# Kernel optimization log

Hardware: AMD Instinct MI355X
Metric: run time of the kernel (lower is better)

The kernel has to match this reference:

```python
import jax, jax.numpy as jnp
import numpy as np

D_SCALE = 1000.0  # quantization scale for the int32 motion-magnitude depth key


def _forward_warp_max_motion(im0, flow, eps):
    """Depth-tested forward splatting (Sanchez et al. 2013, Alg. 3, max-motion variant).

    Each source pixel is bilinearly splatted to the 4 integer neighbors of its
    flow-displaced target. A scatter-max on quantized motion magnitude acts as the
    depth test; only contributions whose motion equals the per-pixel max are
    accumulated (deterministic two-pass version of the atomic CUDA kernel).
    """
    B, C, H, W = im0.shape
    fx, fy = flow[..., 0], flow[..., 1]
    x = jnp.arange(W, dtype=flow.dtype)[None, None, :] + fx  # [B,H,W] target x
    y = jnp.arange(H, dtype=flow.dtype)[None, :, None] + fy  # [B,H,W] target y
    x0 = jnp.floor(x)
    y0 = jnp.floor(y)
    ax = x - x0  # fractional parts -> bilinear weights
    ay = y - y0
    x0i = x0.astype(jnp.int32)
    y0i = y0.astype(jnp.int32)
    corners = [
        (x0i,     y0i,     (1.0 - ax) * (1.0 - ay)),
        (x0i + 1, y0i,     ax * (1.0 - ay)),
        (x0i,     y0i + 1, (1.0 - ax) * ay),
        (x0i + 1, y0i + 1, ax * ay),
    ]
    d = jnp.round(jnp.sqrt(fx * fx + fy * fy) * D_SCALE).astype(jnp.int32)  # [B,H,W]
    boff = (jnp.arange(B, dtype=jnp.int32) * (H * W))[:, None, None]
    idxs, ws, ds = [], [], []
    for tx, ty, w in corners:
        valid = (tx >= 0) & (tx < W) & (ty >= 0) & (ty < H)
        idx = jnp.where(valid, boff + ty * W + tx, 0)
        idxs.append(idx.reshape(-1))
        ws.append(jnp.where(valid, w, 0.0).reshape(-1))
        ds.append(jnp.where(valid, d, -1).reshape(-1))
    idx = jnp.concatenate(idxs)        # [4*B*H*W]
    wv = jnp.concatenate(ws)
    dv = jnp.concatenate(ds)
    N = B * H * W
    # pass 1: scatter-max depth buffer (init 0, as in the torch code)
    dbuf = jnp.zeros(N, jnp.int32).at[idx].max(dv)
    # pass 2: accumulate only depth-test winners
    win = (dv >= 0) & (dv == dbuf[idx])
    w_eff = jnp.where(win, wv, 0.0)
    wght = jnp.zeros(N, im0.dtype).at[idx].add(w_eff)  # kernel adds w per channel then /C == w once
    src = im0.transpose(1, 0, 2, 3).reshape(C, N)      # [C, N]
    vals = jnp.tile(src, (1, 4)) * w_eff[None, :]      # [C, 4N], corner-major matches idx
    im1buf = jnp.zeros((C, N), im0.dtype).at[:, idx].add(vals)
    wght_b = wght.reshape(B, 1, H, W)
    im1buf_b = im1buf.reshape(C, B, H, W).transpose(1, 0, 2, 3)
    im1 = im1buf_b / jnp.clip(wght_b, eps, None)
    disocclusions = (wght_b == 0).astype(im0.dtype)
    return im1, disocclusions, dbuf.reshape(B, 1, H, W)


def setup_inputs() -> dict:
    key = jax.random.key(0)
    k1, k2 = jax.random.split(key)
    B, C, H, W = 4, 3, 1080, 1920
    im0 = jax.random.uniform(k1, (B, C, H, W), dtype=jnp.float32)
    flow = jax.random.normal(k2, (B, H, W, 2), dtype=jnp.float32) * 20.0  # ~20 px motions
    return {"im0": im0, "flow": flow}


def reference(im0, flow):
    eps = 1e-05
    im1, _, _ = _forward_warp_max_motion(im0, flow, eps)
    return im1
```

## Files before the change

kernel.cpp:

```cpp
#include <hip/hip_runtime.h>

static constexpr int B = 4, C = 3, H = 1080, W = 1920;
static constexpr int HW = H * W;
static constexpr int NPIX = B * HW;
static constexpr int BLOCK = 256;

static constexpr int TW = 32, TH = 32;
static constexpr int TPX = TW * TH;
static constexpr int TXN = W / TW;
static constexpr int TYN = (H + TH - 1) / TH;
static constexpr int NT = TXN * TYN;
static constexpr int CAP = 1536;
static constexpr int OFL_CAP = 65536;
static constexpr int BPB = HW / BLOCK;

__device__ __forceinline__ int depth_key(float fx, float fy) {
    float m2 = __fadd_rn(__fmul_rn(fx, fx), __fmul_rn(fy, fy));
    return (int)rintf(__fmul_rn(sqrtf(m2), 1000.0f));
}

__global__ __launch_bounds__(BLOCK) void k_bin(const float2* __restrict__ flow,
                                               int* __restrict__ cnt,
                                               float4* __restrict__ bin,
                                               int* __restrict__ ofl_cnt,
                                               int* __restrict__ ofl_i,
                                               int* __restrict__ ofl_t,
                                               int* __restrict__ dbuf) {
    __shared__ int hcnt[NT];
    __shared__ int hbase[NT];
    const int tid = threadIdx.x;

    const int b = blockIdx.x / BPB;
    const int i = blockIdx.x * BLOCK + tid;
    const float2 f = flow[i];

    for (int j = tid; j < NT; j += BLOCK) hcnt[j] = 0;
    __syncthreads();

    const int pix = i - b * HW;
    const int h = pix / W;
    const int w = pix - h * W;
    const float x = (float)w + f.x;
    const float y = (float)h + f.y;
    const int x0 = (int)floorf(x);
    const int y0 = (int)floorf(y);
    const int d = depth_key(f.x, f.y);

    int tl[4], rk[4]; int ntl = 0;
    #pragma unroll
    for (int dy = 0; dy < 2; ++dy) {
        int cy = y0 + dy;
        if ((unsigned)cy >= (unsigned)H) continue;
        #pragma unroll
        for (int dx = 0; dx < 2; ++dx) {
            int cx = x0 + dx;
            if ((unsigned)cx >= (unsigned)W) continue;
            int t = (cy >> 5) * TXN + (cx >> 5);
            bool dup = false;
            for (int k = 0; k < ntl; ++k) dup |= (tl[k] == t);
            if (dup) continue;
            tl[ntl] = t;
            rk[ntl] = atomicAdd(&hcnt[t], 1);
            ++ntl;
        }
    }
    __syncthreads();

    for (int j = tid; j < NT; j += BLOCK) {
        int c = hcnt[j];
        if (c > 0) hbase[j] = atomicAdd(&cnt[b * NT + j], c);
    }
    __syncthreads();

    const float4 entry = make_float4(x, y, __int_as_float(pix), __int_as_float(d));
    bool did_depth_fb = false;
    for (int k = 0; k < ntl; ++k) {
        int t = tl[k];
        int slot = hbase[t] + rk[k];
        if (slot < CAP) {
            bin[(size_t)(b * NT + t) * CAP + slot] = entry;
        } else {
            int pos = atomicAdd(ofl_cnt, 1);
            if (pos < OFL_CAP) { ofl_i[pos] = i; ofl_t[pos] = t; }
            if (!did_depth_fb) {
                did_depth_fb = true;
                #pragma unroll
                for (int yy = 0; yy < 2; ++yy) {
                    int cy2 = y0 + yy;
                    if ((unsigned)cy2 >= (unsigned)H) continue;
                    #pragma unroll
                    for (int xx = 0; xx < 2; ++xx) {
                        int cx2 = x0 + xx;
                        if ((unsigned)cx2 >= (unsigned)W) continue;
                        atomicMax(&dbuf[b * HW + cy2 * W + cx2], d);
                    }
                }
            }
        }
    }
}

__global__ __launch_bounds__(BLOCK, 8) void k_tile(const float* __restrict__ im0,
                                                   const int* __restrict__ cnt,
                                                   const float4* __restrict__ bin,
                                                   const int* __restrict__ ofl_cnt,
                                                   int* __restrict__ dbuf,
                                                   float* __restrict__ wght,
                                                   float* __restrict__ out) {
    __shared__ int    dmax[TPX];
    __shared__ float4 accv[TPX];
    float* accf = (float*)accv;
    const int tid = threadIdx.x;
    const int bx = blockIdx.x, by = blockIdx.y, b = blockIdx.z;
    const int tx0 = bx * TW, ty0 = by * TH;
    const int t = by * TXN + bx;
    const bool have_ofl = (*ofl_cnt) > 0;
    int* db = dbuf + (size_t)b * HW;

    for (int i = tid; i < TPX; i += BLOCK) {
        int gy = ty0 + (i >> 5), gx = tx0 + (i & 31);
        dmax[i] = (have_ofl && gy < H) ? db[gy * W + gx] : 0;
        accv[i] = make_float4(0.0f, 0.0f, 0.0f, 0.0f);
    }
    __syncthreads();

    const int n = min(cnt[b * NT + t], CAP);
    const float4* mybin = bin + (size_t)(b * NT + t) * CAP;

    for (int e = tid; e < n; e += BLOCK) {
        float4 en = mybin[e];
        int x0 = (int)floorf(en.x);
        int y0 = (int)floorf(en.y);
        int d = __float_as_int(en.w);
        #pragma unroll
        for (int dy = 0; dy < 2; ++dy) {
            int cy = y0 + dy;
            if ((cy >> 5) != by || cy >= H) continue;
            #pragma unroll
            for (int dx = 0; dx < 2; ++dx) {
                int cx = x0 + dx;
                if ((cx >> 5) != bx) continue;
                atomicMax(&dmax[((cy - ty0) << 5) + (cx - tx0)], d);
            }
        }
    }
    __syncthreads();

    if (have_ofl) {
        for (int i = tid; i < TPX; i += BLOCK) {
            int gy = ty0 + (i >> 5), gx = tx0 + (i & 31);
            if (gy < H) db[gy * W + gx] = dmax[i];
        }
    }

    const float* ib = im0 + (size_t)b * C * HW;
    for (int e = tid; e < n; e += BLOCK) {
        float4 en = mybin[e];
        float x0f = floorf(en.x), y0f = floorf(en.y);
        int x0 = (int)x0f, y0 = (int)y0f;
        float ax = __fsub_rn(en.x, x0f);
        float ay = __fsub_rn(en.y, y0f);
        int pix = __float_as_int(en.z);
        int d   = __float_as_int(en.w);
        float wxv[2] = { __fsub_rn(1.0f, ax), ax };
        float wyv[2] = { __fsub_rn(1.0f, ay), ay };
        int   locs[4]; float lw[4]; int nw = 0;
        #pragma unroll
        for (int dy = 0; dy < 2; ++dy) {
            int cy = y0 + dy;
            if ((cy >> 5) != by || cy >= H) continue;
            #pragma unroll
            for (int dx = 0; dx < 2; ++dx) {
                int cx = x0 + dx;
                if ((cx >> 5) != bx) continue;
                int loc = ((cy - ty0) << 5) + (cx - tx0);
                if (dmax[loc] != d) continue;
                locs[nw] = loc;
                lw[nw] = __fmul_rn(wxv[dx], wyv[dy]);
                ++nw;
            }
        }
        if (nw) {
            float c0 = ib[pix];
            float c1 = ib[pix + HW];
            float c2 = ib[pix + 2 * HW];
            for (int k = 0; k < nw; ++k) {
                int p = locs[k]; float wg = lw[k];
                atomicAdd(&accf[4 * p + 0], wg);
                atomicAdd(&accf[4 * p + 1], __fmul_rn(c0, wg));
                atomicAdd(&accf[4 * p + 2], __fmul_rn(c1, wg));
                atomicAdd(&accf[4 * p + 3], __fmul_rn(c2, wg));
            }
        }
    }
    __syncthreads();

    float* ob = out + (size_t)b * C * HW;
    float* wb = wght + (size_t)b * HW;
    for (int i = tid; i < TPX; i += BLOCK) {
        int gy = ty0 + (i >> 5), gx = tx0 + (i & 31);
        if (gy >= H) continue;
        int g = gy * W + gx;
        float4 a = accv[i];
        if (have_ofl) {
            wb[g] = a.x;
            ob[g] = a.y; ob[g + HW] = a.z; ob[g + 2 * HW] = a.w;
        } else {
            float wv = fmaxf(a.x, 1e-5f);
            ob[g]          = __fdiv_rn(a.y, wv);
            ob[g + HW]     = __fdiv_rn(a.z, wv);
            ob[g + 2 * HW] = __fdiv_rn(a.w, wv);
        }
    }
}

__global__ __launch_bounds__(BLOCK) void k_accum_ofl(const float* __restrict__ im0,
                                                     const float2* __restrict__ flow,
                                                     const int* __restrict__ ofl_cnt,
                                                     const int* __restrict__ ofl_i,
                                                     const int* __restrict__ ofl_t,
                                                     const int* __restrict__ dbuf,
                                                     float* __restrict__ wght,
                                                     float* __restrict__ out) {
    int k = blockIdx.x * BLOCK + threadIdx.x;
    int n = min(*ofl_cnt, OFL_CAP);
    if (k >= n) return;
    int i = ofl_i[k], t = ofl_t[k];
    int b = i / HW;
    int pix = i - b * HW;
    int h = pix / W, w = pix - h * W;
    int bx = t % TXN, by = t / TXN;
    float2 f = flow[i];
    float x = (float)w + f.x;
    float y = (float)h + f.y;
    float x0f = floorf(x), y0f = floorf(y);
    int x0 = (int)x0f, y0 = (int)y0f;
    float ax = __fsub_rn(x, x0f);
    float ay = __fsub_rn(y, y0f);
    int d = depth_key(f.x, f.y);
    const float* src = im0 + (size_t)b * C * HW + pix;
    float c0 = src[0], c1 = src[HW], c2 = src[2 * HW];
    float wxv[2] = { __fsub_rn(1.0f, ax), ax };
    float wyv[2] = { __fsub_rn(1.0f, ay), ay };
    #pragma unroll
    for (int dy = 0; dy < 2; ++dy) {
        int cy = y0 + dy;
        if ((cy >> 5) != by || cy >= H) continue;
        #pragma unroll
        for (int dx = 0; dx < 2; ++dx) {
            int cx = x0 + dx;
            if ((cx >> 5) != bx) continue;
            int idx = b * HW + cy * W + cx;
            if (dbuf[idx] != d) continue;
            float wg = __fmul_rn(wxv[dx], wyv[dy]);
            atomicAdd(&wght[idx], wg);
            float* o = out + (size_t)b * C * HW + cy * W + cx;
            atomicAdd(&o[0],      __fmul_rn(c0, wg));
            atomicAdd(&o[HW],     __fmul_rn(c1, wg));
            atomicAdd(&o[2 * HW], __fmul_rn(c2, wg));
        }
    }
}

__global__ __launch_bounds__(BLOCK) void k_norm(float* __restrict__ out,
                                                const float* __restrict__ wght,
                                                const int* __restrict__ ofl_cnt) {
    if (*ofl_cnt == 0) return;
    for (int i = blockIdx.x * BLOCK + threadIdx.x; i < NPIX;
         i += gridDim.x * BLOCK) {
        int b = i / HW;
        int pix = i - b * HW;
        float wv = fmaxf(wght[i], 1e-5f);
        float* o = out + (size_t)b * C * HW + pix;
        o[0]      = __fdiv_rn(o[0], wv);
        o[HW]     = __fdiv_rn(o[HW], wv);
        o[2 * HW] = __fdiv_rn(o[2 * HW], wv);
    }
}

extern "C" void kernel_launch(void* const* d_in, const int* in_sizes, int n_in,
                              void* d_out, int out_size, void* d_ws, size_t ws_size,
                              hipStream_t stream) {
    const float*  im0  = (const float*)d_in[0];
    const float2* flow = (const float2*)d_in[1];
    float* out = (float*)d_out;

    char* ws = (char*)d_ws;
    float4* bin = (float4*)ws;
    const size_t bin_bytes = (size_t)B * NT * CAP * sizeof(float4);
    int*   dbuf    = (int*)(ws + bin_bytes);
    float* wght    = (float*)(ws + bin_bytes + (size_t)NPIX * 4);
    int*   cnt     = (int*)(ws + bin_bytes + (size_t)NPIX * 8);
    int*   ofl_cnt = cnt + B * NT;
    int*   ofl_i   = ofl_cnt + 1;
    int*   ofl_t   = ofl_i + OFL_CAP;

    hipMemsetAsync(dbuf, 0, (size_t)NPIX * 4, stream);
    hipMemsetAsync(cnt, 0, (size_t)(B * NT + 1) * 4, stream);

    int lgrid = NPIX / BLOCK;
    dim3 tgrid(TXN, TYN, B);

    k_bin      <<<lgrid, BLOCK, 0, stream>>>(flow, cnt, bin, ofl_cnt, ofl_i, ofl_t, dbuf);
    k_tile     <<<tgrid, BLOCK, 0, stream>>>(im0, cnt, bin, ofl_cnt, dbuf, wght, out);
    k_accum_ofl<<<OFL_CAP / BLOCK, BLOCK, 0, stream>>>(im0, flow, ofl_cnt, ofl_i, ofl_t, dbuf, wght, out);
    k_norm     <<<2048, BLOCK, 0, stream>>>(out, wght, ofl_cnt);
}
```

Measured before the change: 453.0 us.

## Process multiple pixels per thread in binning and register-cache tile entries

New measurement: 428.4 us. 1.06x faster.

```diff
diff --git a/kernel.cpp b/kernel.cpp
--- a/kernel.cpp
+++ b/kernel.cpp
@@ -11,12 +11,32 @@
 static constexpr int TYN = (H + TH - 1) / TH;
 static constexpr int NT = TXN * TYN;
 static constexpr int CAP = 1536;
+static constexpr int EPT = CAP / BLOCK;
 static constexpr int OFL_CAP = 65536;
-static constexpr int BPB = HW / BLOCK;
+
+static constexpr int PPT = 4;
+static constexpr int BPIX = BLOCK * PPT;
+static constexpr int BPB = HW / BPIX;
 
 __device__ __forceinline__ int depth_key(float fx, float fy) {
     float m2 = __fadd_rn(__fmul_rn(fx, fx), __fmul_rn(fy, fy));
     return (int)rintf(__fmul_rn(sqrtf(m2), 1000.0f));
+}
+
+__device__ __forceinline__ void merge_depth(int* __restrict__ dbuf, int bHW,
+                                            float x, float y, int d) {
+    int x0 = (int)floorf(x), y0 = (int)floorf(y);
+    #pragma unroll
+    for (int yy = 0; yy < 2; ++yy) {
+        int cy = y0 + yy;
+        if ((unsigned)cy >= (unsigned)H) continue;
+        #pragma unroll
+        for (int xx = 0; xx < 2; ++xx) {
+            int cx = x0 + xx;
+            if ((unsigned)cx >= (unsigned)W) continue;
+            atomicMax(&dbuf[bHW + cy * W + cx], d);
+        }
+    }
 }
 
 __global__ __launch_bounds__(BLOCK) void k_bin(const float2* __restrict__ flow,
@@ -29,40 +49,45 @@
     __shared__ int hcnt[NT];
     __shared__ int hbase[NT];
     const int tid = threadIdx.x;
-
     const int b = blockIdx.x / BPB;
-    const int i = blockIdx.x * BLOCK + tid;
-    const float2 f = flow[i];
+    const int gbase = blockIdx.x * BPIX + tid;
+
+    float2 f[PPT];
+    #pragma unroll
+    for (int k = 0; k < PPT; ++k) f[k] = flow[gbase + k * BLOCK];
 
     for (int j = tid; j < NT; j += BLOCK) hcnt[j] = 0;
     __syncthreads();
 
-    const int pix = i - b * HW;
-    const int h = pix / W;
-    const int w = pix - h * W;
-    const float x = (float)w + f.x;
-    const float y = (float)h + f.y;
-    const int x0 = (int)floorf(x);
-    const int y0 = (int)floorf(y);
-    const int d = depth_key(f.x, f.y);
-
-    int tl[4], rk[4]; int ntl = 0;
-    #pragma unroll
-    for (int dy = 0; dy < 2; ++dy) {
-        int cy = y0 + dy;
-        if ((unsigned)cy >= (unsigned)H) continue;
-        #pragma unroll
-        for (int dx = 0; dx < 2; ++dx) {
-            int cx = x0 + dx;
-            if ((unsigned)cx >= (unsigned)W) continue;
-            int t = (cy >> 5) * TXN + (cx >> 5);
-            bool dup = false;
-            for (int k = 0; k < ntl; ++k) dup |= (tl[k] == t);
-            if (dup) continue;
-            tl[ntl] = t;
-            rk[ntl] = atomicAdd(&hcnt[t], 1);
-            ++ntl;
-        }
+    float xs[PPT], ys[PPT];
+    int dd[PPT];
+    int ta[PPT], tb[PPT], tc[PPT], td[PPT];
+    int ra[PPT], rb[PPT], rc[PPT], rd[PPT];
+    #pragma unroll
+    for (int k = 0; k < PPT; ++k) {
+        const int i = gbase + k * BLOCK;
+        const int pix = i - b * HW;
+        const int h = pix / W;
+        const int w = pix - h * W;
+        const float x = (float)w + f[k].x;
+        const float y = (float)h + f[k].y;
+        xs[k] = x; ys[k] = y;
+        dd[k] = depth_key(f[k].x, f[k].y);
+        const int x0 = (int)floorf(x), y0 = (int)floorf(y);
+        const int x1 = x0 + 1, y1 = y0 + 1;
+        const bool vx0 = (unsigned)x0 < (unsigned)W, vx1 = (unsigned)x1 < (unsigned)W;
+        const bool vy0 = (unsigned)y0 < (unsigned)H, vy1 = (unsigned)y1 < (unsigned)H;
+        const int cx0 = x0 >> 5, cx1 = x1 >> 5;
+        const int cy0 = y0 >> 5, cy1 = y1 >> 5;
+        const bool dupx = (cx1 == cx0), dupy = (cy1 == cy0);
+        ta[k] = (vy0 && vx0)                   ? cy0 * TXN + cx0 : -1;
+        tb[k] = (vy0 && vx1 && !dupx)          ? cy0 * TXN + cx1 : -1;
+        tc[k] = (vy1 && vx0 && !dupy)          ? cy1 * TXN + cx0 : -1;
+        td[k] = (vy1 && vx1 && !dupx && !dupy) ? cy1 * TXN + cx1 : -1;
+        ra[k] = (ta[k] >= 0) ? atomicAdd(&hcnt[ta[k]], 1) : 0;
+        rb[k] = (tb[k] >= 0) ? atomicAdd(&hcnt[tb[k]], 1) : 0;
+        rc[k] = (tc[k] >= 0) ? atomicAdd(&hcnt[tc[k]], 1) : 0;
+        rd[k] = (td[k] >= 0) ? atomicAdd(&hcnt[td[k]], 1) : 0;
     }
     __syncthreads();
 
@@ -72,41 +97,42 @@
     }
     __syncthreads();
 
-    const float4 entry = make_float4(x, y, __int_as_float(pix), __int_as_float(d));
-    bool did_depth_fb = false;
-    for (int k = 0; k < ntl; ++k) {
-        int t = tl[k];
-        int slot = hbase[t] + rk[k];
-        if (slot < CAP) {
-            bin[(size_t)(b * NT + t) * CAP + slot] = entry;
-        } else {
-            int pos = atomicAdd(ofl_cnt, 1);
-            if (pos < OFL_CAP) { ofl_i[pos] = i; ofl_t[pos] = t; }
-            if (!did_depth_fb) {
-                did_depth_fb = true;
-                #pragma unroll
-                for (int yy = 0; yy < 2; ++yy) {
-                    int cy2 = y0 + yy;
-                    if ((unsigned)cy2 >= (unsigned)H) continue;
-                    #pragma unroll
-                    for (int xx = 0; xx < 2; ++xx) {
-                        int cx2 = x0 + xx;
-                        if ((unsigned)cx2 >= (unsigned)W) continue;
-                        atomicMax(&dbuf[b * HW + cy2 * W + cx2], d);
-                    }
-                }
-            }
-        }
-    }
-}
-
-__global__ __launch_bounds__(BLOCK, 8) void k_tile(const float* __restrict__ im0,
-                                                   const int* __restrict__ cnt,
-                                                   const float4* __restrict__ bin,
-                                                   const int* __restrict__ ofl_cnt,
-                                                   int* __restrict__ dbuf,
-                                                   float* __restrict__ wght,
-                                                   float* __restrict__ out) {
+    #pragma unroll
+    for (int k = 0; k < PPT; ++k) {
+        const int i = gbase + k * BLOCK;
+        const int pix = i - b * HW;
+        const float4 entry = make_float4(xs[k], ys[k],
+                                         __int_as_float(pix), __int_as_float(dd[k]));
+        bool fb = false;
+        #define EMIT(T, R)                                                     \
+            if ((T) >= 0) {                                                    \
+                int slot = hbase[T] + (R);                                     \
+                if (slot < CAP) {                                              \
+                    bin[(size_t)(b * NT + (T)) * CAP + slot] = entry;          \
+                } else {                                                       \
+                    int pos = atomicAdd(ofl_cnt, 1);                           \
+                    if (pos < OFL_CAP) { ofl_i[pos] = i; ofl_t[pos] = (T); }   \
+                    if (!fb) {                                                 \
+                        fb = true;                                             \
+                        merge_depth(dbuf, b * HW, xs[k], ys[k], dd[k]);        \
+                    }                                                          \
+                }                                                              \
+            }
+        EMIT(ta[k], ra[k])
+        EMIT(tb[k], rb[k])
+        EMIT(tc[k], rc[k])
+        EMIT(td[k], rd[k])
+        #undef EMIT
+    }
+}
+
+__global__ __launch_bounds__(BLOCK) void k_tile(const float* __restrict__ im0,
+                                                const int* __restrict__ cnt,
+                                                const float4* __restrict__ bin,
+                                                const int* __restrict__ ofl_cnt,
+                                                int* __restrict__ dbuf,
+                                                float* __restrict__ wght,
+                                                float* __restrict__ out) {
     __shared__ int    dmax[TPX];
     __shared__ float4 accv[TPX];
     float* accf = (float*)accv;
@@ -117,6 +143,17 @@
     const bool have_ofl = (*ofl_cnt) > 0;
     int* db = dbuf + (size_t)b * HW;
 
+    const int n = min(cnt[b * NT + t], CAP);
+    const float4* mybin = bin + (size_t)(b * NT + t) * CAP;
+
+    const int emax = max(n - 1, 0);
+    float4 eA[EPT];
+    #pragma unroll
+    for (int k = 0; k < EPT; ++k) {
+        int e = min(tid + k * BLOCK, emax);
+        eA[k] = mybin[e];
+    }
+
     for (int i = tid; i < TPX; i += BLOCK) {
         int gy = ty0 + (i >> 5), gx = tx0 + (i & 31);
         dmax[i] = (have_ofl && gy < H) ? db[gy * W + gx] : 0;
@@ -124,23 +161,23 @@
     }
     __syncthreads();
 
-    const int n = min(cnt[b * NT + t], CAP);
-    const float4* mybin = bin + (size_t)(b * NT + t) * CAP;
-
-    for (int e = tid; e < n; e += BLOCK) {
-        float4 en = mybin[e];
-        int x0 = (int)floorf(en.x);
-        int y0 = (int)floorf(en.y);
-        int d = __float_as_int(en.w);
-        #pragma unroll
-        for (int dy = 0; dy < 2; ++dy) {
-            int cy = y0 + dy;
-            if ((cy >> 5) != by || cy >= H) continue;
+    #pragma unroll
+    for (int k = 0; k < EPT; ++k) {
+        if (tid + k * BLOCK < n) {
+            float4 en = eA[k];
+            int x0 = (int)floorf(en.x);
+            int y0 = (int)floorf(en.y);
+            int d = __float_as_int(en.w);
             #pragma unroll
-            for (int dx = 0; dx < 2; ++dx) {
-                int cx = x0 + dx;
-                if ((cx >> 5) != bx) continue;
-                atomicMax(&dmax[((cy - ty0) << 5) + (cx - tx0)], d);
+            for (int dy = 0; dy < 2; ++dy) {
+                int cy = y0 + dy;
+                if ((cy >> 5) != by || cy >= H) continue;
+                #pragma unroll
+                for (int dx = 0; dx < 2; ++dx) {
+                    int cx = x0 + dx;
+                    if ((cx >> 5) != bx) continue;
+                    atomicMax(&dmax[((cy - ty0) << 5) + (cx - tx0)], d);
+                }
             }
         }
     }
@@ -154,42 +191,63 @@
     }
 
     const float* ib = im0 + (size_t)b * C * HW;
-    for (int e = tid; e < n; e += BLOCK) {
-        float4 en = mybin[e];
-        float x0f = floorf(en.x), y0f = floorf(en.y);
-        int x0 = (int)x0f, y0 = (int)y0f;
-        float ax = __fsub_rn(en.x, x0f);
-        float ay = __fsub_rn(en.y, y0f);
-        int pix = __float_as_int(en.z);
-        int d   = __float_as_int(en.w);
-        float wxv[2] = { __fsub_rn(1.0f, ax), ax };
-        float wyv[2] = { __fsub_rn(1.0f, ay), ay };
-        int   locs[4]; float lw[4]; int nw = 0;
-        #pragma unroll
-        for (int dy = 0; dy < 2; ++dy) {
-            int cy = y0 + dy;
-            if ((cy >> 5) != by || cy >= H) continue;
+    int   wmask[EPT];
+    float c0[EPT], c1[EPT], c2[EPT];
+    #pragma unroll
+    for (int k = 0; k < EPT; ++k) {
+        wmask[k] = 0;
+        if (tid + k * BLOCK < n) {
+            float4 en = eA[k];
+            int x0 = (int)floorf(en.x);
+            int y0 = (int)floorf(en.y);
+            int d = __float_as_int(en.w);
+            int m = 0;
             #pragma unroll
-            for (int dx = 0; dx < 2; ++dx) {
-                int cx = x0 + dx;
-                if ((cx >> 5) != bx) continue;
-                int loc = ((cy - ty0) << 5) + (cx - tx0);
-                if (dmax[loc] != d) continue;
-                locs[nw] = loc;
-                lw[nw] = __fmul_rn(wxv[dx], wyv[dy]);
-                ++nw;
-            }
-        }
-        if (nw) {
-            float c0 = ib[pix];
-            float c1 = ib[pix + HW];
-            float c2 = ib[pix + 2 * HW];
-            for (int k = 0; k < nw; ++k) {
-                int p = locs[k]; float wg = lw[k];
-                atomicAdd(&accf[4 * p + 0], wg);
-                atomicAdd(&accf[4 * p + 1], __fmul_rn(c0, wg));
-                atomicAdd(&accf[4 * p + 2], __fmul_rn(c1, wg));
-                atomicAdd(&accf[4 * p + 3], __fmul_rn(c2, wg));
+            for (int dy = 0; dy < 2; ++dy) {
+                int cy = y0 + dy;
+                if ((cy >> 5) != by || cy >= H) continue;
+                #pragma unroll
+                for (int dx = 0; dx < 2; ++dx) {
+                    int cx = x0 + dx;
+                    if ((cx >> 5) != bx) continue;
+                    if (dmax[((cy - ty0) << 5) + (cx - tx0)] == d)
+                        m |= 1 << (dy * 2 + dx);
+                }
+            }
+            wmask[k] = m;
+            if (m) {
+                int pix = __float_as_int(en.z);
+                c0[k] = ib[pix];
+                c1[k] = ib[pix + HW];
+                c2[k] = ib[pix + 2 * HW];
+            }
+        }
+    }
+
+    #pragma unroll
+    for (int k = 0; k < EPT; ++k) {
+        int m = wmask[k];
+        if (m) {
+            float4 en = eA[k];
+            float x0f = floorf(en.x), y0f = floorf(en.y);
+            int x0 = (int)x0f, y0 = (int)y0f;
+            float ax = __fsub_rn(en.x, x0f);
+            float ay = __fsub_rn(en.y, y0f);
+            float wx[2] = { __fsub_rn(1.0f, ax), ax };
+            float wy[2] = { __fsub_rn(1.0f, ay), ay };
+            #pragma unroll
+            for (int dy = 0; dy < 2; ++dy) {
+                #pragma unroll
+                for (int dx = 0; dx < 2; ++dx) {
+                    if (m & (1 << (dy * 2 + dx))) {
+                        int loc = ((y0 + dy - ty0) << 5) + (x0 + dx - tx0);
+                        float wg = __fmul_rn(wx[dx], wy[dy]);
+                        atomicAdd(&accf[4 * loc + 0], wg);
+                        atomicAdd(&accf[4 * loc + 1], __fmul_rn(c0[k], wg));
+                        atomicAdd(&accf[4 * loc + 2], __fmul_rn(c1[k], wg));
+                        atomicAdd(&accf[4 * loc + 3], __fmul_rn(c2[k], wg));
+                    }
+                }
             }
         }
     }
@@ -298,10 +356,10 @@
     hipMemsetAsync(dbuf, 0, (size_t)NPIX * 4, stream);
     hipMemsetAsync(cnt, 0, (size_t)(B * NT + 1) * 4, stream);
 
-    int lgrid = NPIX / BLOCK;
+    int bgrid = NPIX / BPIX;
     dim3 tgrid(TXN, TYN, B);
 
-    k_bin      <<<lgrid, BLOCK, 0, stream>>>(flow, cnt, bin, ofl_cnt, ofl_i, ofl_t, dbuf);
+    k_bin      <<<bgrid, BLOCK, 0, stream>>>(flow, cnt, bin, ofl_cnt, ofl_i, ofl_t, dbuf);
     k_tile     <<<tgrid, BLOCK, 0, stream>>>(im0, cnt, bin, ofl_cnt, dbuf, wght, out);
     k_accum_ofl<<<OFL_CAP / BLOCK, BLOCK, 0, stream>>>(im0, flow, ofl_cnt, ofl_i, ofl_t, dbuf, wght, out);
     k_norm     <<<2048, BLOCK, 0, stream>>>(out, wght, ofl_cnt);
```
